# Kernel tuning notes

Hardware: AMD Instinct MI355X
Metric: run time of the kernel (lower is better)

## Reference

```python
import jax, jax.numpy as jnp
import numpy as np

COST_CLASS = 2.0
COST_BBOX = 5.0
COST_GIOU = 2.0
COST_INNER = 9999.0
FOCAL_ALPHA = 0.25
FOCAL_GAMMA = 2.0
EPS = 1e-8


def box_cxcywh_to_xyxy(b):
    cx, cy, w, h = b[..., 0], b[..., 1], b[..., 2], b[..., 3]
    return jnp.stack([cx - 0.5 * w, cy - 0.5 * h, cx + 0.5 * w, cy + 0.5 * h], axis=-1)


def generalized_box_iou(boxes1, boxes2):
    # boxes in xyxy; boxes1 [N,4], boxes2 [T,4] -> [N,T]
    area1 = (boxes1[:, 2] - boxes1[:, 0]) * (boxes1[:, 3] - boxes1[:, 1])
    area2 = (boxes2[:, 2] - boxes2[:, 0]) * (boxes2[:, 3] - boxes2[:, 1])
    lt = jnp.maximum(boxes1[:, None, :2], boxes2[None, :, :2])
    rb = jnp.minimum(boxes1[:, None, 2:], boxes2[None, :, 2:])
    wh = jnp.clip(rb - lt, 0.0)
    inter = wh[..., 0] * wh[..., 1]
    union = area1[:, None] + area2[None, :] - inter
    iou = inter / union
    # enclosing box
    lt_c = jnp.minimum(boxes1[:, None, :2], boxes2[None, :, :2])
    rb_c = jnp.maximum(boxes1[:, None, 2:], boxes2[None, :, 2:])
    wh_c = jnp.clip(rb_c - lt_c, 0.0)
    area_c = wh_c[..., 0] * wh_c[..., 1]
    return iou - (area_c - union) / area_c


def setup_inputs() -> dict:
    key = jax.random.key(0)
    k1, k2, k3, k4, k5, k6 = jax.random.split(key, 6)
    bs, nq, nc, T = 16, 900, 91, 1024
    return {
        "pred_logits": jax.random.normal(k1, (bs, nq, nc), dtype=jnp.float32),
        "pred_boxes": jax.random.uniform(k2, (bs, nq, 4), dtype=jnp.float32),
        "pred_points": jax.random.uniform(k3, (bs, nq, 2), dtype=jnp.float32),
        "pred_objs": jax.random.normal(k4, (bs, nq, 1), dtype=jnp.float32),
        "tgt_labels": jax.random.randint(k5, (T,), 0, nc, dtype=jnp.int64),
        "tgt_boxes": jax.random.uniform(k6, (T, 4), dtype=jnp.float32),
    }


def reference(pred_logits, pred_boxes, pred_points, pred_objs, tgt_labels, tgt_boxes):
    bs, nq, nc = pred_logits.shape
    out_prob = jax.nn.sigmoid(pred_logits.reshape(bs * nq, nc))       # [N,C]
    out_bbox = pred_boxes.reshape(bs * nq, 4)                          # [N,4]
    out_point = pred_points.reshape(bs * nq, 2)                        # [N,2]
    out_obj = jax.nn.sigmoid(pred_objs.reshape(bs * nq, 1))            # [N,1]
    out_prob = out_prob * out_obj

    # focal classification cost, gathered at target classes -> [N,T]
    neg = (1.0 - FOCAL_ALPHA) * out_prob ** FOCAL_GAMMA * (-jnp.log(1.0 - out_prob + EPS))
    pos = FOCAL_ALPHA * (1.0 - out_prob) ** FOCAL_GAMMA * (-jnp.log(out_prob + EPS))
    cost_class = jnp.take(pos, tgt_labels, axis=1) - jnp.take(neg, tgt_labels, axis=1)

    out_xyxy = box_cxcywh_to_xyxy(out_bbox)
    tgt_xyxy = box_cxcywh_to_xyxy(tgt_boxes)

    # L1 cdist on xyxy boxes -> [N,T]
    cost_bbox = jnp.sum(jnp.abs(out_xyxy[:, None, :] - tgt_xyxy[None, :, :]), axis=-1)

    cost_giou = -generalized_box_iou(out_xyxy, tgt_xyxy)               # [N,T]

    # inner-point cost: 1 if predicted point falls outside target box
    left = out_point[:, 0, None] - tgt_xyxy[None, :, 0]
    top = out_point[:, 1, None] - tgt_xyxy[None, :, 1]
    right = tgt_xyxy[None, :, 2] - out_point[:, 0, None]
    bottom = tgt_xyxy[None, :, 3] - out_point[:, 1, None]
    min_dist = jnp.minimum(jnp.minimum(left, top), jnp.minimum(right, bottom))
    cost_inner = 1.0 - (min_dist >= 0.0).astype(out_prob.dtype)

    C = (COST_BBOX * cost_bbox + COST_CLASS * cost_class
         + COST_GIOU * cost_giou + COST_INNER * cost_inner)
    return C.reshape(bs, nq, -1)
```

## Files before the change

kernel.cpp:

```cpp
#include <hip/hip_runtime.h>
#include <math.h>


#define BN 8
#define BT 256
#define VT 4

__global__ __launch_bounds__(BT) void matcher_kernel(
    const float* __restrict__ logits,
    const float* __restrict__ boxes,
    const float* __restrict__ points,
    const float* __restrict__ objs,
    const int*   __restrict__ labels,
    const float* __restrict__ tboxes,
    float* __restrict__ out,
    int N, int C, int T)
{
    __shared__ float s_tab[96 * BN];
    __shared__ float s_row[BN][8];

    const int tid = threadIdx.x;
    const int rowBase = blockIdx.y * BN;
    const int t0 = tid * VT;

    if (tid < BN) {
        int n = rowBase + tid;
        float4 b = *(const float4*)(boxes + 4 * n);
        float x0 = b.x - 0.5f * b.z;
        float y0 = b.y - 0.5f * b.w;
        float x1 = b.x + 0.5f * b.z;
        float y1 = b.y + 0.5f * b.w;
        s_row[tid][0] = x0;
        s_row[tid][1] = y0;
        s_row[tid][2] = x1;
        s_row[tid][3] = y1;
        float2 p = *(const float2*)(points + 2 * n);
        s_row[tid][4] = p.x;
        s_row[tid][5] = p.y;
        s_row[tid][6] = (x1 - x0) * (y1 - y0);
        s_row[tid][7] = __builtin_amdgcn_rcpf(1.0f + __expf(-objs[n]));
    }
    __syncthreads();

    for (int idx = tid; idx < BN * C; idx += BT) {
        int r = idx / C;
        int c = idx - r * C;
        float lg = logits[(size_t)rowBase * C + idx];
        float ps = __builtin_amdgcn_rcpf(1.0f + __expf(-lg));
        float p = ps * s_row[r][7];
        float omp = 1.0f - p;
        float pos = 0.25f * (omp * omp) * (-__logf(p + 1e-8f));
        float neg = 0.75f * (p * p) * (-__logf(omp + 1e-8f));
        s_tab[c * BN + r] = pos - neg;
    }
    __syncthreads();

    {
        int4 lv = *(const int4*)(labels + t0);
        int lab[VT] = {lv.x, lv.y, lv.z, lv.w};
        float tx0[VT], ty0[VT], tx1[VT], ty1[VT], tarea[VT];
        #pragma unroll
        for (int j = 0; j < VT; ++j) {
            float4 tb = *(const float4*)(tboxes + 4 * (t0 + j));
            tx0[j] = tb.x - 0.5f * tb.z;
            ty0[j] = tb.y - 0.5f * tb.w;
            tx1[j] = tb.x + 0.5f * tb.z;
            ty1[j] = tb.y + 0.5f * tb.w;
            tarea[j] = (tx1[j] - tx0[j]) * (ty1[j] - ty0[j]);
        }

        float cc[VT][BN];
        #pragma unroll
        for (int j = 0; j < VT; ++j) {
            const float4* tp = (const float4*)(s_tab + lab[j] * BN);
            float4 lo = tp[0];
            float4 hi = tp[1];
            cc[j][0] = lo.x; cc[j][1] = lo.y; cc[j][2] = lo.z; cc[j][3] = lo.w;
            cc[j][4] = hi.x; cc[j][5] = hi.y; cc[j][6] = hi.z; cc[j][7] = hi.w;
        }

        float rx0[BN], ry0[BN], rx1[BN], ry1[BN], rpx[BN], rpy[BN], ra1[BN];
        #pragma unroll
        for (int r = 0; r < BN; ++r) {
            float4 ra = *(const float4*)&s_row[r][0];
            float4 rb = *(const float4*)&s_row[r][4];
            rx0[r] = ra.x; ry0[r] = ra.y; rx1[r] = ra.z; ry1[r] = ra.w;
            rpx[r] = rb.x; rpy[r] = rb.y; ra1[r] = rb.z;
        }

        float* obase = out + (size_t)rowBase * T + t0;
        #pragma unroll
        for (int r = 0; r < BN; ++r) {
            float x0 = rx0[r], y0 = ry0[r], x1 = rx1[r], y1 = ry1[r];
            float px = rpx[r], py = rpy[r], a1 = ra1[r];

            float4 res;
            float* resp = (float*)&res;
            #pragma unroll
            for (int j = 0; j < VT; ++j) {
                float l1 = fabsf(x0 - tx0[j]) + fabsf(y0 - ty0[j])
                         + fabsf(x1 - tx1[j]) + fabsf(y1 - ty1[j]);

                float iw = fminf(x1, tx1[j]) - fmaxf(x0, tx0[j]);
                float ih = fminf(y1, ty1[j]) - fmaxf(y0, ty0[j]);
                float inter = fmaxf(iw, 0.0f) * fmaxf(ih, 0.0f);
                float uni = (a1 + tarea[j]) - inter;

                float cw = fmaxf(x1, tx1[j]) - fminf(x0, tx0[j]);
                float ch = fmaxf(y1, ty1[j]) - fminf(y0, ty0[j]);
                float carea = cw * ch;

                float R = __builtin_amdgcn_rcpf(uni * carea);
                float giou = (inter * carea - uni * (carea - uni)) * R;

                float left = px - tx0[j];
                float top = py - ty0[j];
                float right = tx1[j] - px;
                float bottom = ty1[j] - py;
                float mind = fminf(fminf(left, top), fminf(right, bottom));

                float Cv = fmaf(5.0f, l1, fmaf(2.0f, cc[j][r], -2.0f * giou));
                Cv += (mind >= 0.0f) ? 0.0f : 9999.0f;
                resp[j] = Cv;
            }
            *(float4*)(obase + (size_t)r * T) = res;
        }
    }
}

extern "C" void kernel_launch(void* const* d_in, const int* in_sizes, int n_in,
                              void* d_out, int out_size, void* d_ws, size_t ws_size,
                              hipStream_t stream) {
    const float* logits = (const float*)d_in[0];
    const float* boxes  = (const float*)d_in[1];
    const float* points = (const float*)d_in[2];
    const float* objs   = (const float*)d_in[3];
    const int*   labels = (const int*)d_in[4];
    const float* tboxes = (const float*)d_in[5];
    float* out = (float*)d_out;

    int N = in_sizes[1] / 4;
    int T = in_sizes[5] / 4;
    int C = in_sizes[0] / N;

    dim3 grid(1, N / BN);
    matcher_kernel<<<grid, BT, 0, stream>>>(logits, boxes, points, objs,
                                            labels, tboxes, out, N, C, T);
}
```

Baseline: 97.43 us.

## Use nontemporal stores, padded class table, early target loads, and fewer barriers

Writes the output tile with nontemporal vector stores so the write-only cost matrix bypasses cache retention. The class-cost table gets a padded stride of 12 to cut LDS bank conflicts on the label-indexed gathers. Label and target-box loads are hoisted before the first phase to overlap their latency, and the first barrier is removed by computing the object sigmoid per element. The L1 distance is rewritten from the min/max terms, and occupancy is hinted via launch bounds. Recomputing the object sigmoid per element adds redundant transcendental work.

```diff
diff --git a/kernel.cpp b/kernel.cpp
--- a/kernel.cpp
+++ b/kernel.cpp
@@ -5,8 +5,11 @@
 #define BN 8
 #define BT 256
 #define VT 4
+#define TSTRIDE 12
 
-__global__ __launch_bounds__(BT) void matcher_kernel(
+typedef float f32x4 __attribute__((ext_vector_type(4)));
+
+__global__ __launch_bounds__(BT, 4) void matcher_kernel(
     const float* __restrict__ logits,
     const float* __restrict__ boxes,
     const float* __restrict__ points,
@@ -16,12 +19,20 @@
     float* __restrict__ out,
     int N, int C, int T)
 {
-    __shared__ float s_tab[96 * BN];
-    __shared__ float s_row[BN][8];
+    __shared__ __align__(16) float s_tab[96 * TSTRIDE];
+    __shared__ __align__(16) float s_row[BN][8];
 
     const int tid = threadIdx.x;
     const int rowBase = blockIdx.y * BN;
     const int t0 = tid * VT;
+
+    int4 lv = *(const int4*)(labels + t0);
+    float4 tbs[VT];
+    tbs[0] = *(const float4*)(tboxes + 4 * (t0 + 0));
+    tbs[1] = *(const float4*)(tboxes + 4 * (t0 + 1));
+    tbs[2] = *(const float4*)(tboxes + 4 * (t0 + 2));
+    tbs[3] = *(const float4*)(tboxes + 4 * (t0 + 3));
+    int lab[VT] = {lv.x, lv.y, lv.z, lv.w};
 
     if (tid < BN) {
         int n = rowBase + tid;
@@ -38,93 +49,87 @@
         s_row[tid][4] = p.x;
         s_row[tid][5] = p.y;
         s_row[tid][6] = (x1 - x0) * (y1 - y0);
-        s_row[tid][7] = __builtin_amdgcn_rcpf(1.0f + __expf(-objs[n]));
+        s_row[tid][7] = 0.0f;
     }
-    __syncthreads();
 
     for (int idx = tid; idx < BN * C; idx += BT) {
         int r = idx / C;
         int c = idx - r * C;
         float lg = logits[(size_t)rowBase * C + idx];
+        float po = __builtin_amdgcn_rcpf(1.0f + __expf(-objs[rowBase + r]));
         float ps = __builtin_amdgcn_rcpf(1.0f + __expf(-lg));
-        float p = ps * s_row[r][7];
+        float p = ps * po;
         float omp = 1.0f - p;
         float pos = 0.25f * (omp * omp) * (-__logf(p + 1e-8f));
         float neg = 0.75f * (p * p) * (-__logf(omp + 1e-8f));
-        s_tab[c * BN + r] = pos - neg;
+        s_tab[c * TSTRIDE + r] = pos - neg;
     }
     __syncthreads();
 
-    {
-        int4 lv = *(const int4*)(labels + t0);
-        int lab[VT] = {lv.x, lv.y, lv.z, lv.w};
-        float tx0[VT], ty0[VT], tx1[VT], ty1[VT], tarea[VT];
+    float tx0[VT], ty0[VT], tx1[VT], ty1[VT], tarea[VT];
+    #pragma unroll
+    for (int j = 0; j < VT; ++j) {
+        float4 tb = tbs[j];
+        tx0[j] = tb.x - 0.5f * tb.z;
+        ty0[j] = tb.y - 0.5f * tb.w;
+        tx1[j] = tb.x + 0.5f * tb.z;
+        ty1[j] = tb.y + 0.5f * tb.w;
+        tarea[j] = (tx1[j] - tx0[j]) * (ty1[j] - ty0[j]);
+    }
+
+    float cc[VT][BN];
+    #pragma unroll
+    for (int j = 0; j < VT; ++j) {
+        const float* tp = s_tab + lab[j] * TSTRIDE;
+        float4 lo = *(const float4*)(tp);
+        float4 hi = *(const float4*)(tp + 4);
+        cc[j][0] = lo.x; cc[j][1] = lo.y; cc[j][2] = lo.z; cc[j][3] = lo.w;
+        cc[j][4] = hi.x; cc[j][5] = hi.y; cc[j][6] = hi.z; cc[j][7] = hi.w;
+    }
+
+    float* obase = out + (size_t)rowBase * T + t0;
+    #pragma unroll
+    for (int r = 0; r < BN; ++r) {
+        float4 ra = *(const float4*)&s_row[r][0];
+        float4 rb = *(const float4*)&s_row[r][4];
+        float x0 = ra.x, y0 = ra.y, x1 = ra.z, y1 = ra.w;
+        float px = rb.x, py = rb.y, a1 = rb.z;
+
+        f32x4 res;
         #pragma unroll
         for (int j = 0; j < VT; ++j) {
-            float4 tb = *(const float4*)(tboxes + 4 * (t0 + j));
-            tx0[j] = tb.x - 0.5f * tb.z;
-            ty0[j] = tb.y - 0.5f * tb.w;
-            tx1[j] = tb.x + 0.5f * tb.z;
-            ty1[j] = tb.y + 0.5f * tb.w;
-            tarea[j] = (tx1[j] - tx0[j]) * (ty1[j] - ty0[j]);
+            float mnx0 = fminf(x0, tx0[j]), mxx0 = fmaxf(x0, tx0[j]);
+            float mny0 = fminf(y0, ty0[j]), mxy0 = fmaxf(y0, ty0[j]);
+            float mnx1 = fminf(x1, tx1[j]), mxx1 = fmaxf(x1, tx1[j]);
+            float mny1 = fminf(y1, ty1[j]), mxy1 = fmaxf(y1, ty1[j]);
+
+            float iw = mnx1 - mxx0;
+            float ih = mny1 - mxy0;
+            float cw = mxx1 - mnx0;
+            float ch = mxy1 - mny0;
+
+            float l1 = (cw - iw) + (ch - ih);
+
+            float inter = fmaxf(iw, 0.0f) * fmaxf(ih, 0.0f);
+            float uni = (a1 + tarea[j]) - inter;
+            float carea = cw * ch;
+
+            float R = __builtin_amdgcn_rcpf(uni * carea);
+            float giou = fmaf(inter, carea, -(uni * (carea - uni))) * R;
+
+            float left = px - tx0[j];
+            float top = py - ty0[j];
+            float right = tx1[j] - px;
+            float bottom = ty1[j] - py;
+            float mind = fminf(fminf(left, top), fminf(right, bottom));
+
+            float inner = (mind >= 0.0f) ? 0.0f : 9999.0f;
+            float Cv = fmaf(5.0f, l1,
+                       fmaf(2.0f, cc[j][r],
+                       fmaf(-2.0f, giou, inner)));
+            res[j] = Cv;
         }
-
-        float cc[VT][BN];
-        #pragma unroll
-        for (int j = 0; j < VT; ++j) {
-            const float4* tp = (const float4*)(s_tab + lab[j] * BN);
-            float4 lo = tp[0];
-            float4 hi = tp[1];
-            cc[j][0] = lo.x; cc[j][1] = lo.y; cc[j][2] = lo.z; cc[j][3] = lo.w;
-            cc[j][4] = hi.x; cc[j][5] = hi.y; cc[j][6] = hi.z; cc[j][7] = hi.w;
-        }
-
-        float rx0[BN], ry0[BN], rx1[BN], ry1[BN], rpx[BN], rpy[BN], ra1[BN];
-        #pragma unroll
-        for (int r = 0; r < BN; ++r) {
-            float4 ra = *(const float4*)&s_row[r][0];
-            float4 rb = *(const float4*)&s_row[r][4];
-            rx0[r] = ra.x; ry0[r] = ra.y; rx1[r] = ra.z; ry1[r] = ra.w;
-            rpx[r] = rb.x; rpy[r] = rb.y; ra1[r] = rb.z;
-        }
-
-        float* obase = out + (size_t)rowBase * T + t0;
-        #pragma unroll
-        for (int r = 0; r < BN; ++r) {
-            float x0 = rx0[r], y0 = ry0[r], x1 = rx1[r], y1 = ry1[r];
-            float px = rpx[r], py = rpy[r], a1 = ra1[r];
-
-            float4 res;
-            float* resp = (float*)&res;
-            #pragma unroll
-            for (int j = 0; j < VT; ++j) {
-                float l1 = fabsf(x0 - tx0[j]) + fabsf(y0 - ty0[j])
-                         + fabsf(x1 - tx1[j]) + fabsf(y1 - ty1[j]);
-
-                float iw = fminf(x1, tx1[j]) - fmaxf(x0, tx0[j]);
-                float ih = fminf(y1, ty1[j]) - fmaxf(y0, ty0[j]);
-                float inter = fmaxf(iw, 0.0f) * fmaxf(ih, 0.0f);
-                float uni = (a1 + tarea[j]) - inter;
-
-                float cw = fmaxf(x1, tx1[j]) - fminf(x0, tx0[j]);
-                float ch = fmaxf(y1, ty1[j]) - fminf(y0, ty0[j]);
-                float carea = cw * ch;
-
-                float R = __builtin_amdgcn_rcpf(uni * carea);
-                float giou = (inter * carea - uni * (carea - uni)) * R;
-
-                float left = px - tx0[j];
-                float top = py - ty0[j];
-                float right = tx1[j] - px;
-                float bottom = ty1[j] - py;
-                float mind = fminf(fminf(left, top), fminf(right, bottom));
-
-                float Cv = fmaf(5.0f, l1, fmaf(2.0f, cc[j][r], -2.0f * giou));
-                Cv += (mind >= 0.0f) ? 0.0f : 9999.0f;
-                resp[j] = Cv;
-            }
-            *(float4*)(obase + (size_t)r * T) = res;
-        }
+        __builtin_nontemporal_store(res, (f32x4*)(obase + (size_t)r * T));
     }
 }
 
```

Result: no change. 95.68 us (-1.8%).
